# Kernel optimization log

Hardware: AMD Instinct MI355X
Metric: run time of the kernel (lower is better)

## Reference

```python
import jax, jax.numpy as jnp
import numpy as np

N_HEADS, N_KV, HEAD_DIM, D_MODEL, T_MAX = 16, 4, 64, 1024, 2048
GROUPS = N_HEADS // N_KV
EPS = 1e-6


def _rms_norm(x, w):
    # RMSNorm over last dim (head_dim), computed in fp32 like the torch module
    xf = x.astype(jnp.float32)
    r = jax.lax.rsqrt(jnp.mean(xf * xf, axis=-1, keepdims=True) + EPS)
    return (xf * r).astype(x.dtype) * w


def _apply_rope(x, cos, sin):
    # x: (B, H, T, D); cos/sin: (T_max, D/2)
    T = x.shape[2]
    c = cos[:T][None, None]  # (1,1,T,D/2)
    s = sin[:T][None, None]
    x1, x2 = jnp.split(x, 2, axis=-1)
    return jnp.concatenate([x1 * c - x2 * s, x2 * c + x1 * s], axis=-1)


def setup_inputs() -> dict:
    key = jax.random.key(0)
    ks = jax.random.split(key, 8)
    B, T = 2, 2048
    x = jax.random.normal(ks[0], (B, T, D_MODEL), dtype=jnp.float32)
    # realistic RoPE tables
    theta = 10000.0
    inv_freq = 1.0 / (theta ** (np.arange(0, HEAD_DIM, 2, dtype=np.float32) / HEAD_DIM))
    t = np.arange(T_MAX, dtype=np.float32)
    freqs = np.outer(t, inv_freq)  # (T_max, D/2)
    cos = jnp.asarray(np.cos(freqs))
    sin = jnp.asarray(np.sin(freqs))
    sd = 0.02
    wq = jax.random.normal(ks[1], (N_HEADS * HEAD_DIM, D_MODEL), dtype=jnp.float32) * sd
    wk = jax.random.normal(ks[2], (N_KV * HEAD_DIM, D_MODEL), dtype=jnp.float32) * sd
    wv = jax.random.normal(ks[3], (N_KV * HEAD_DIM, D_MODEL), dtype=jnp.float32) * sd
    wo = jax.random.normal(ks[4], (D_MODEL, N_HEADS * HEAD_DIM), dtype=jnp.float32) * sd
    qn_w = jnp.ones((HEAD_DIM,), dtype=jnp.float32)
    kn_w = jnp.ones((HEAD_DIM,), dtype=jnp.float32)
    return {"x": x, "cos": cos, "sin": sin, "wq": wq, "wk": wk, "wv": wv,
            "wo": wo, "qn_w": qn_w, "kn_w": kn_w}


def reference(x, cos, sin, wq, wk, wv, wo, qn_w, kn_w):
    B, T, _ = x.shape
    scale = HEAD_DIM ** -0.5
    # projections (torch Linear: y = x @ W.T)
    q = (x @ wq.T).reshape(B, T, N_HEADS, HEAD_DIM).transpose(0, 2, 1, 3)
    k = (x @ wk.T).reshape(B, T, N_KV, HEAD_DIM).transpose(0, 2, 1, 3)
    v = (x @ wv.T).reshape(B, T, N_KV, HEAD_DIM).transpose(0, 2, 1, 3)
    # qk RMSNorm
    q = _rms_norm(q, qn_w)
    k = _rms_norm(k, kn_w)
    # RoPE
    q = _apply_rope(q, cos, sin)
    k = _apply_rope(k, cos, sin)
    # GQA expansion: query head h uses kv head h // GROUPS
    k = jnp.repeat(k, GROUPS, axis=1)  # (B, H, T, D)
    v = jnp.repeat(v, GROUPS, axis=1)
    # causal SDPA
    scores = jnp.einsum('bhqd,bhkd->bhqk', q, k) * scale
    causal = jnp.tril(jnp.ones((T, T), dtype=bool))
    scores = jnp.where(causal, scores, jnp.finfo(scores.dtype).min)
    p = jax.nn.softmax(scores, axis=-1)
    out = jnp.einsum('bhqk,bhkd->bhqd', p, v)
    out = out.transpose(0, 2, 1, 3).reshape(B, T, N_HEADS * HEAD_DIM)
    return out @ wo.T
```

## Files before the change

kernel.cpp:

```cpp
#include <hip/hip_runtime.h>


typedef __bf16 bf16;
typedef __attribute__((ext_vector_type(4))) __bf16 bf16x4;
typedef __attribute__((ext_vector_type(8))) __bf16 bf16x8;
typedef __attribute__((ext_vector_type(4))) float f32x4;

#define MFMA(a, b, c) __builtin_amdgcn_mfma_f32_16x16x32_bf16((a), (b), (c), 0, 0, 0)
#define GLOAD_LDS16(g, l)                                        \
  __builtin_amdgcn_global_load_lds(                              \
      (const __attribute__((address_space(1))) void*)(g),        \
      (__attribute__((address_space(3))) void*)(l), 16, 0, 0)

__device__ __forceinline__ bool is_bf16_input(const void* cosRaw) {
  return ((const unsigned short*)cosRaw)[0] == 0x3F80;
}
__device__ __forceinline__ float rdval(const void* p, int idx, bool isbf) {
  return isbf ? (float)((const bf16*)p)[idx] : ((const float*)p)[idx];
}

__global__ __launch_bounds__(256) void convert_kernel(
    const void* __restrict__ x, const void* __restrict__ wq,
    const void* __restrict__ wk, const void* __restrict__ wv,
    const void* __restrict__ wo, bf16* __restrict__ dx,
    bf16* __restrict__ dw, const void* __restrict__ cosraw) {
  const bool isbf = is_bf16_input(cosraw);
  const int c = (int)blockIdx.x * 256 + (int)threadIdx.x;
  const void* src;
  int off;
  bf16* dst;
  int dc;
  if (c < 524288)      { src = x;  off = c;          dst = dx; dc = c; }
  else if (c < 655360) { src = wq; off = c - 524288; dst = dw; dc = c - 524288; }
  else if (c < 688128) { src = wk; off = c - 655360; dst = dw; dc = c - 524288; }
  else if (c < 720896) { src = wv; off = c - 688128; dst = dw; dc = c - 524288; }
  else                 { src = wo; off = c - 720896; dst = dw; dc = c - 524288; }
  bf16x8 o;
  if (isbf) {
    o = ((const bf16x8*)src)[off];
  } else {
    const float4* fp = (const float4*)src + (size_t)off * 2;
    float4 f0 = fp[0];
    float4 f1 = fp[1];
    o[0] = (bf16)f0.x; o[1] = (bf16)f0.y; o[2] = (bf16)f0.z; o[3] = (bf16)f0.w;
    o[4] = (bf16)f1.x; o[5] = (bf16)f1.y; o[6] = (bf16)f1.z; o[7] = (bf16)f1.w;
  }
  ((bf16x8*)dst)[dc] = o;
}

__global__ __launch_bounds__(256, 3) void proj_kernel(
    const bf16* __restrict__ xb, const bf16* __restrict__ wqb,
    const bf16* __restrict__ wkb, const bf16* __restrict__ wvb,
    bf16* __restrict__ qp, bf16* __restrict__ kp, bf16* __restrict__ vt,
    const void* __restrict__ cosraw, const void* __restrict__ sinraw,
    const void* __restrict__ qnraw, const void* __restrict__ knraw) {
  __shared__ bf16 As[128 * 64];
  __shared__ bf16 Bs[64 * 64];

  const int idx = (int)blockIdx.x;
  const int xcd = idx & 7;
  const int jj = idx >> 3;
  const int mb = (jj & 3) * 8 + xcd;
  const int nb = jj >> 2;
  const int n0 = nb * 64;
  const int m0 = mb * 128;

  const int tid = threadIdx.x;
  const int wave = tid >> 6;
  const int lane = tid & 63;
  const int q16 = lane & 15;
  const int quad = lane >> 4;
  const int srow = lane >> 3;
  const int csrc = (lane & 7) ^ srow;
  const int x7 = q16 & 7;

  const bf16* wsrc;
  int nr0;
  if (nb < 16)      { wsrc = wqb; nr0 = n0; }
  else if (nb < 20) { wsrc = wkb; nr0 = n0 - 1024; }
  else              { wsrc = wvb; nr0 = n0 - 1280; }

  f32x4 acc[2][4];
#pragma unroll
  for (int mf = 0; mf < 2; ++mf)
#pragma unroll
    for (int nt = 0; nt < 4; ++nt) acc[mf][nt] = (f32x4){0.f, 0.f, 0.f, 0.f};

  for (int kt = 0; kt < 16; ++kt) {
    const int ko = kt * 64;
#pragma unroll
    for (int i = 0; i < 4; ++i) {
      int rb = wave * 32 + i * 8;
      GLOAD_LDS16(&xb[(size_t)(m0 + rb + srow) * 1024 + ko + csrc * 8],
                  &As[rb * 64]);
    }
#pragma unroll
    for (int i = 0; i < 2; ++i) {
      int rb = wave * 16 + i * 8;
      GLOAD_LDS16(&wsrc[(size_t)(nr0 + rb + srow) * 1024 + ko + csrc * 8],
                  &Bs[rb * 64]);
    }
    __syncthreads();

    bf16x8 a[2][2], bfr[4][2];
#pragma unroll
    for (int mf = 0; mf < 2; ++mf) {
      const bf16* rp = &As[(wave * 32 + mf * 16 + q16) * 64];
      a[mf][0] = *(const bf16x8*)&rp[(quad ^ x7) * 8];
      a[mf][1] = *(const bf16x8*)&rp[((quad + 4) ^ x7) * 8];
    }
#pragma unroll
    for (int nt = 0; nt < 4; ++nt) {
      const bf16* rp = &Bs[(nt * 16 + q16) * 64];
      bfr[nt][0] = *(const bf16x8*)&rp[(quad ^ x7) * 8];
      bfr[nt][1] = *(const bf16x8*)&rp[((quad + 4) ^ x7) * 8];
    }
#pragma unroll
    for (int nt = 0; nt < 4; ++nt)
#pragma unroll
      for (int mf = 0; mf < 2; ++mf) {
        acc[mf][nt] = MFMA(a[mf][0], bfr[nt][0], acc[mf][nt]);
        acc[mf][nt] = MFMA(a[mf][1], bfr[nt][1], acc[mf][nt]);
      }
    __syncthreads();
  }

  if (nb < 20) {
    const bool isbf = is_bf16_input(cosraw);
    const void* nwp = (nb < 16) ? qnraw : knraw;
    const float osc = (nb < 16) ? 0.125f : 1.0f;
    float wd[4];
#pragma unroll
    for (int nt = 0; nt < 4; ++nt) wd[nt] = rdval(nwp, nt * 16 + q16, isbf);

#pragma unroll
    for (int mf = 0; mf < 2; ++mf) {
#pragma unroll
      for (int r = 0; r < 4; ++r) {
        float p = acc[mf][0][r] * acc[mf][0][r] + acc[mf][1][r] * acc[mf][1][r] +
                  acc[mf][2][r] * acc[mf][2][r] + acc[mf][3][r] * acc[mf][3][r];
#pragma unroll
        for (int off = 8; off >= 1; off >>= 1) p += __shfl_xor(p, off);
        float rms = rsqrtf(p * (1.0f / 64.0f) + 1e-6f);

        int row = m0 + wave * 32 + mf * 16 + quad * 4 + r;
        int t = row & 2047;
        float c0 = rdval(cosraw, t * 32 + q16, isbf);
        float c1 = rdval(cosraw, t * 32 + 16 + q16, isbf);
        float s0 = rdval(sinraw, t * 32 + q16, isbf);
        float s1 = rdval(sinraw, t * 32 + 16 + q16, isbf);

        float v0 = acc[mf][0][r] * rms * wd[0];
        float v1 = acc[mf][1][r] * rms * wd[1];
        float v2 = acc[mf][2][r] * rms * wd[2];
        float v3 = acc[mf][3][r] * rms * wd[3];

        bf16* op = (nb < 16) ? &qp[(size_t)row * 1024 + nb * 64]
                             : &kp[(size_t)row * 256 + (nb - 16) * 64];
        op[0 * 16 + q16] = (bf16)((v0 * c0 - v2 * s0) * osc);
        op[1 * 16 + q16] = (bf16)((v1 * c1 - v3 * s1) * osc);
        op[2 * 16 + q16] = (bf16)((v2 * c0 + v0 * s0) * osc);
        op[3 * 16 + q16] = (bf16)((v3 * c1 + v1 * s1) * osc);
      }
    }
  } else {
    const int vh = nb - 20;
    const int b = m0 >> 11;
    const int tbase = m0 & 2047;
#pragma unroll
    for (int mf = 0; mf < 2; ++mf)
#pragma unroll
      for (int nt = 0; nt < 4; ++nt)
#pragma unroll
        for (int r = 0; r < 4; ++r)
          As[(wave * 32 + mf * 16 + quad * 4 + r) * 64 + nt * 16 + q16] =
              (bf16)acc[mf][nt][r];
    __syncthreads();
#pragma unroll
    for (int rep = 0; rep < 4; ++rep) {
      int c = tid + 256 * rep;
      int d = c >> 4;
      int t8 = (c & 15) * 8;
      bf16x8 pk;
#pragma unroll
      for (int j = 0; j < 8; ++j) pk[j] = As[(t8 + j) * 64 + d];
      *(bf16x8*)&vt[(((size_t)(b * 4 + vh)) * 64 + d) * 2048 + tbase + t8] = pk;
    }
  }
}

__global__ __launch_bounds__(256, 4) void flash_kernel(
    const bf16* __restrict__ qp, const bf16* __restrict__ kp,
    const bf16* __restrict__ vt, bf16* __restrict__ attn) {
  const int qblk = blockIdx.z ? 31 - (int)blockIdx.x : (int)blockIdx.x;
  const int h = blockIdx.y;
  const int b = blockIdx.z;
  const int kvh = h >> 2;
  const int tid = threadIdx.x;
  const int wave = tid >> 6;
  const int lane = tid & 63;
  const int q16 = lane & 15;
  const int quad = lane >> 4;
  const int r7 = q16 & 7;
  const int t0 = qblk * 64 + wave * 16;

  __shared__ bf16 Ks[2][64 * 64];
  __shared__ bf16 Vs[2][64 * 64];
  __shared__ bf16 Pl[4][16 * 32];

  const bf16* qrow = qp + (((size_t)(b * 2048 + t0 + q16)) * 16 + h) * 64;
  bf16x8 qa0 = *(const bf16x8*)(qrow + quad * 8);
  bf16x8 qa1 = *(const bf16x8*)(qrow + 32 + quad * 8);

  bf16x8 ones;
#pragma unroll
  for (int j = 0; j < 8; ++j) ones[j] = (bf16)1.0f;

  f32x4 O[4], l4;
#pragma unroll
  for (int nt = 0; nt < 4; ++nt) O[nt] = (f32x4){0.f, 0.f, 0.f, 0.f};
  l4 = (f32x4){0.f, 0.f, 0.f, 0.f};

  const int ntile = qblk + 1;

  bf16x8 kr[2], vr[2];
  const int cr = tid * 2;
  const int krow = cr >> 3;
  const size_t kgbase = (((size_t)(b * 2048) + krow) * 4 + kvh) * 64;
  const size_t vgbase = ((size_t)(b * 4 + kvh) * 64 + krow) * 2048;

  auto gload = [&](int tk) {
#pragma unroll
    for (int rep = 0; rep < 2; ++rep) {
      int ch = (cr + rep) & 7;
      kr[rep] = *(const bf16x8*)&kp[kgbase + (size_t)(tk * 64) * 256 + ch * 8];
      vr[rep] = *(const bf16x8*)&vt[vgbase + tk * 64 + ch * 8];
    }
  };
  auto swrite = [&](int bb) {
#pragma unroll
    for (int rep = 0; rep < 2; ++rep) {
      int ch = (cr + rep) & 7;
      int pos = (ch ^ (krow & 7)) * 8;
      *(bf16x8*)&Ks[bb][krow * 64 + pos] = kr[rep];
      *(bf16x8*)&Vs[bb][krow * 64 + pos] = vr[rep];
    }
  };

  gload(0);

  for (int t = 0; t < ntile; ++t) {
    const int bb = t & 1;
    const int kbase = t * 64;
    swrite(bb);
    __syncthreads();
    if (t + 1 < ntile) gload(t + 1);

    f32x4 s[4];
#pragma unroll
    for (int kt = 0; kt < 4; ++kt) {
      const bf16* kr0 = &Ks[bb][(kt * 16 + q16) * 64];
      bf16x8 kb0 = *(const bf16x8*)&kr0[(quad ^ r7) * 8];
      bf16x8 kb1 = *(const bf16x8*)&kr0[((quad + 4) ^ r7) * 8];
      f32x4 z = (f32x4){0.f, 0.f, 0.f, 0.f};
      z = MFMA(kb0, qa0, z);
      z = MFMA(kb1, qa1, z);
      s[kt] = z;
    }

    if (kbase + 63 > t0) {
      const int q = t0 + q16;
#pragma unroll
      for (int kt = 0; kt < 4; ++kt) {
        int jt = kbase + kt * 16 + quad * 4;
#pragma unroll
        for (int r = 0; r < 4; ++r)
          if (jt + r > q) s[kt][r] = -1e30f;
      }
    }

#pragma unroll
    for (int kt = 0; kt < 4; ++kt)
#pragma unroll
      for (int r = 0; r < 4; ++r) s[kt][r] = __expf(s[kt][r] - 9.0f);

#pragma unroll
    for (int kh = 0; kh < 2; ++kh) {
#pragma unroll
      for (int ct = 0; ct < 2; ++ct) {
        const int kt = kh * 2 + ct;
        bf16x4 pk;
#pragma unroll
        for (int r = 0; r < 4; ++r) pk[r] = (bf16)s[kt][r];
        *(bf16x4*)&Pl[wave][q16 * 32 + ((ct * 4 + quad) ^ (q16 & 6)) * 4] = pk;
      }
      bf16x8 pa = *(const bf16x8*)&Pl[wave][q16 * 32 + ((quad * 2) ^ (q16 & 6)) * 4];
#pragma unroll
      for (int nt = 0; nt < 4; ++nt) {
        const bf16* vr0 = &Vs[bb][(nt * 16 + q16) * 64];
        bf16x8 vb = *(const bf16x8*)&vr0[((kh * 4 + quad) ^ r7) * 8];
        O[nt] = MFMA(pa, vb, O[nt]);
      }
      l4 = MFMA(pa, ones, l4);
    }
  }

  float inv[4];
#pragma unroll
  for (int r = 0; r < 4; ++r) inv[r] = 1.0f / l4[r];
#pragma unroll
  for (int nt = 0; nt < 4; ++nt)
#pragma unroll
    for (int r = 0; r < 4; ++r) {
      size_t o = (((size_t)(b * 2048 + t0 + quad * 4 + r)) * 16 + h) * 64 +
                 nt * 16 + q16;
      attn[o] = (bf16)(O[nt][r] * inv[r]);
    }
}

__global__ __launch_bounds__(256, 6) void gemm_o_kernel(
    const bf16* __restrict__ A, const bf16* __restrict__ W,
    void* __restrict__ C, const void* __restrict__ cosraw) {
  __shared__ bf16 As[64 * 64];
  __shared__ bf16 Bs[64 * 64];

  const int idx = (int)blockIdx.x;
  const int xcd = idx & 7;
  const int jj = idx >> 3;
  const int mb = (jj & 7) * 8 + xcd;
  const int nb = jj >> 3;
  const int n0 = nb * 64;
  const int m0 = mb * 64;

  const int tid = threadIdx.x;
  const int wave = tid >> 6;
  const int lane = tid & 63;
  const int q16 = lane & 15;
  const int quad = lane >> 4;
  const int srow = lane >> 3;
  const int csrc = (lane & 7) ^ srow;
  const int wm = wave * 16;
  const int x7 = q16 & 7;
  const bool isbf = is_bf16_input(cosraw);

  f32x4 acc[4];
#pragma unroll
  for (int nt = 0; nt < 4; ++nt) acc[nt] = (f32x4){0.f, 0.f, 0.f, 0.f};

  for (int kt = 0; kt < 16; ++kt) {
    const int ko = kt * 64;
#pragma unroll
    for (int i = 0; i < 2; ++i) {
      int rb = wave * 16 + i * 8;
      GLOAD_LDS16(&A[(size_t)(m0 + rb + srow) * 1024 + ko + csrc * 8],
                  &As[rb * 64]);
      GLOAD_LDS16(&W[(size_t)(n0 + rb + srow) * 1024 + ko + csrc * 8],
                  &Bs[rb * 64]);
    }
    __syncthreads();

    bf16x8 a0, a1, bfr[4][2];
    {
      const bf16* rp = &As[(wm + q16) * 64];
      a0 = *(const bf16x8*)&rp[(quad ^ x7) * 8];
      a1 = *(const bf16x8*)&rp[((quad + 4) ^ x7) * 8];
    }
#pragma unroll
    for (int nt = 0; nt < 4; ++nt) {
      const bf16* rp = &Bs[(nt * 16 + q16) * 64];
      bfr[nt][0] = *(const bf16x8*)&rp[(quad ^ x7) * 8];
      bfr[nt][1] = *(const bf16x8*)&rp[((quad + 4) ^ x7) * 8];
    }
#pragma unroll
    for (int nt = 0; nt < 4; ++nt) {
      acc[nt] = MFMA(a0, bfr[nt][0], acc[nt]);
      acc[nt] = MFMA(a1, bfr[nt][1], acc[nt]);
    }
    __syncthreads();
  }

#pragma unroll
  for (int nt = 0; nt < 4; ++nt)
#pragma unroll
    for (int r = 0; r < 4; ++r) {
      size_t idx2 = (size_t)(m0 + wm + quad * 4 + r) * 1024 + n0 + nt * 16 + q16;
      if (isbf) ((bf16*)C)[idx2] = (bf16)acc[nt][r];
      else      ((float*)C)[idx2] = acc[nt][r];
    }
}

extern "C" void kernel_launch(void* const* d_in, const int* in_sizes, int n_in,
                              void* d_out, int out_size, void* d_ws, size_t ws_size,
                              hipStream_t stream) {
  bf16* qp = (bf16*)d_ws;
  bf16* kp = qp + (size_t)4194304;
  bf16* vt = kp + (size_t)1048576;
  bf16* at = vt + (size_t)1048576;
  bf16* xb = at + (size_t)4194304;
  bf16* dw = xb + (size_t)4194304;

  bf16* wqb = dw;
  bf16* wkb = dw + (size_t)1048576;
  bf16* wvb = dw + (size_t)1310720;
  bf16* wob = dw + (size_t)1572864;

  convert_kernel<<<3328, 256, 0, stream>>>(
      d_in[0], d_in[3], d_in[4], d_in[5], d_in[6], xb, dw, d_in[1]);

  proj_kernel<<<768, 256, 0, stream>>>(
      xb, wqb, wkb, wvb, qp, kp, vt,
      d_in[1], d_in[2], d_in[7], d_in[8]);

  flash_kernel<<<dim3(32, 16, 2), 256, 0, stream>>>(qp, kp, vt, at);

  gemm_o_kernel<<<1024, 256, 0, stream>>>(at, wob, d_out, d_in[1]);
}
```

Baseline: 155.7 us.

## Share K/V tiles across two adjacent query blocks per 512-thread flash block

The flash attention kernel now launches 512-thread blocks, with each half handling one of two adjacent 64-row query blocks and both halves sharing the same double-buffered K/V shared-memory tiles. This halves the number of K/V global loads per query row and halves the grid size, while each thread now loads one chunk instead of two. The lower query group sits idle, apart from barriers, during the last KV tile. Larger blocks may reduce occupancy and add synchronisation cost.

```diff
diff --git a/kernel.cpp b/kernel.cpp
--- a/kernel.cpp
+++ b/kernel.cpp
@@ -189,24 +189,30 @@
   }
 }
 
-__global__ __launch_bounds__(256, 4) void flash_kernel(
+__global__ __launch_bounds__(512, 4) void flash_kernel(
     const bf16* __restrict__ qp, const bf16* __restrict__ kp,
     const bf16* __restrict__ vt, bf16* __restrict__ attn) {
-  const int qblk = blockIdx.z ? 31 - (int)blockIdx.x : (int)blockIdx.x;
-  const int h = blockIdx.y;
-  const int b = blockIdx.z;
+  const int x = (int)blockIdx.x;
+  const int h = (int)blockIdx.y;
+  const int b = (int)blockIdx.z;
+  const int p = b ? 15 - x : x;
   const int kvh = h >> 2;
-  const int tid = threadIdx.x;
+  const int tid = (int)threadIdx.x;
   const int wave = tid >> 6;
+  const int g = wave >> 2;
+  const int w4 = wave & 3;
   const int lane = tid & 63;
   const int q16 = lane & 15;
   const int quad = lane >> 4;
   const int r7 = q16 & 7;
-  const int t0 = qblk * 64 + wave * 16;
+  const int qblk = 2 * p + g;
+  const int t0 = qblk * 64 + w4 * 16;
+  const int NT = 2 * p + 2;
+  const int myNT = qblk + 1;
 
   __shared__ bf16 Ks[2][64 * 64];
   __shared__ bf16 Vs[2][64 * 64];
-  __shared__ bf16 Pl[4][16 * 32];
+  __shared__ bf16 Pl[8][16 * 32];
 
   const bf16* qrow = qp + (((size_t)(b * 2048 + t0 + q16)) * 16 + h) * 64;
   bf16x8 qa0 = *(const bf16x8*)(qrow + quad * 8);
@@ -221,87 +227,80 @@
   for (int nt = 0; nt < 4; ++nt) O[nt] = (f32x4){0.f, 0.f, 0.f, 0.f};
   l4 = (f32x4){0.f, 0.f, 0.f, 0.f};
 
-  const int ntile = qblk + 1;
-
-  bf16x8 kr[2], vr[2];
-  const int cr = tid * 2;
-  const int krow = cr >> 3;
+  bf16x8 kr, vr;
+  const int krow = tid >> 3;
+  const int ch = tid & 7;
   const size_t kgbase = (((size_t)(b * 2048) + krow) * 4 + kvh) * 64;
   const size_t vgbase = ((size_t)(b * 4 + kvh) * 64 + krow) * 2048;
 
   auto gload = [&](int tk) {
-#pragma unroll
-    for (int rep = 0; rep < 2; ++rep) {
-      int ch = (cr + rep) & 7;
-      kr[rep] = *(const bf16x8*)&kp[kgbase + (size_t)(tk * 64) * 256 + ch * 8];
-      vr[rep] = *(const bf16x8*)&vt[vgbase + tk * 64 + ch * 8];
-    }
+    kr = *(const bf16x8*)&kp[kgbase + (size_t)(tk * 64) * 256 + ch * 8];
+    vr = *(const bf16x8*)&vt[vgbase + tk * 64 + ch * 8];
   };
   auto swrite = [&](int bb) {
-#pragma unroll
-    for (int rep = 0; rep < 2; ++rep) {
-      int ch = (cr + rep) & 7;
-      int pos = (ch ^ (krow & 7)) * 8;
-      *(bf16x8*)&Ks[bb][krow * 64 + pos] = kr[rep];
-      *(bf16x8*)&Vs[bb][krow * 64 + pos] = vr[rep];
-    }
+    int pos = (ch ^ (krow & 7)) * 8;
+    *(bf16x8*)&Ks[bb][krow * 64 + pos] = kr;
+    *(bf16x8*)&Vs[bb][krow * 64 + pos] = vr;
   };
 
   gload(0);
 
-  for (int t = 0; t < ntile; ++t) {
+  for (int t = 0; t < NT; ++t) {
     const int bb = t & 1;
     const int kbase = t * 64;
     swrite(bb);
     __syncthreads();
-    if (t + 1 < ntile) gload(t + 1);
-
-    f32x4 s[4];
-#pragma unroll
-    for (int kt = 0; kt < 4; ++kt) {
-      const bf16* kr0 = &Ks[bb][(kt * 16 + q16) * 64];
-      bf16x8 kb0 = *(const bf16x8*)&kr0[(quad ^ r7) * 8];
-      bf16x8 kb1 = *(const bf16x8*)&kr0[((quad + 4) ^ r7) * 8];
-      f32x4 z = (f32x4){0.f, 0.f, 0.f, 0.f};
-      z = MFMA(kb0, qa0, z);
-      z = MFMA(kb1, qa1, z);
-      s[kt] = z;
-    }
-
-    if (kbase + 63 > t0) {
-      const int q = t0 + q16;
+    if (t + 1 < NT) gload(t + 1);
+
+    if (t < myNT) {
+      f32x4 s[4];
 #pragma unroll
       for (int kt = 0; kt < 4; ++kt) {
-        int jt = kbase + kt * 16 + quad * 4;
-#pragma unroll
-        for (int r = 0; r < 4; ++r)
-          if (jt + r > q) s[kt][r] = -1e30f;
+        const bf16* kr0 = &Ks[bb][(kt * 16 + q16) * 64];
+        bf16x8 kb0 = *(const bf16x8*)&kr0[(quad ^ r7) * 8];
+        bf16x8 kb1 = *(const bf16x8*)&kr0[((quad + 4) ^ r7) * 8];
+        f32x4 z = (f32x4){0.f, 0.f, 0.f, 0.f};
+        z = MFMA(kb0, qa0, z);
+        z = MFMA(kb1, qa1, z);
+        s[kt] = z;
       }
-    }
-
-#pragma unroll
-    for (int kt = 0; kt < 4; ++kt)
-#pragma unroll
-      for (int r = 0; r < 4; ++r) s[kt][r] = __expf(s[kt][r] - 9.0f);
-
-#pragma unroll
-    for (int kh = 0; kh < 2; ++kh) {
-#pragma unroll
-      for (int ct = 0; ct < 2; ++ct) {
-        const int kt = kh * 2 + ct;
-        bf16x4 pk;
-#pragma unroll
-        for (int r = 0; r < 4; ++r) pk[r] = (bf16)s[kt][r];
-        *(bf16x4*)&Pl[wave][q16 * 32 + ((ct * 4 + quad) ^ (q16 & 6)) * 4] = pk;
+
+      if (kbase + 63 > t0) {
+        const int q = t0 + q16;
+#pragma unroll
+        for (int kt = 0; kt < 4; ++kt) {
+          int jt = kbase + kt * 16 + quad * 4;
+#pragma unroll
+          for (int r = 0; r < 4; ++r)
+            if (jt + r > q) s[kt][r] = -1e30f;
+        }
       }
-      bf16x8 pa = *(const bf16x8*)&Pl[wave][q16 * 32 + ((quad * 2) ^ (q16 & 6)) * 4];
-#pragma unroll
-      for (int nt = 0; nt < 4; ++nt) {
-        const bf16* vr0 = &Vs[bb][(nt * 16 + q16) * 64];
-        bf16x8 vb = *(const bf16x8*)&vr0[((kh * 4 + quad) ^ r7) * 8];
-        O[nt] = MFMA(pa, vb, O[nt]);
+
+#pragma unroll
+      for (int kt = 0; kt < 4; ++kt)
+#pragma unroll
+        for (int r = 0; r < 4; ++r) s[kt][r] = __expf(s[kt][r] - 9.0f);
+
+#pragma unroll
+      for (int kh = 0; kh < 2; ++kh) {
+#pragma unroll
+        for (int ct = 0; ct < 2; ++ct) {
+          const int kt = kh * 2 + ct;
+          bf16x4 pk;
+#pragma unroll
+          for (int r = 0; r < 4; ++r) pk[r] = (bf16)s[kt][r];
+          *(bf16x4*)&Pl[wave][q16 * 32 + ((ct * 4 + quad) ^ (q16 & 6)) * 4] = pk;
+        }
+        bf16x8 pa =
+            *(const bf16x8*)&Pl[wave][q16 * 32 + ((quad * 2) ^ (q16 & 6)) * 4];
+#pragma unroll
+        for (int nt = 0; nt < 4; ++nt) {
+          const bf16* vr0 = &Vs[bb][(nt * 16 + q16) * 64];
+          bf16x8 vb = *(const bf16x8*)&vr0[((kh * 4 + quad) ^ r7) * 8];
+          O[nt] = MFMA(pa, vb, O[nt]);
+        }
+        l4 = MFMA(pa, ones, l4);
       }
-      l4 = MFMA(pa, ones, l4);
     }
   }
 
@@ -411,7 +410,7 @@
       xb, wqb, wkb, wvb, qp, kp, vt,
       d_in[1], d_in[2], d_in[7], d_in[8]);
 
-  flash_kernel<<<dim3(32, 16, 2), 256, 0, stream>>>(qp, kp, vt, at);
+  flash_kernel<<<dim3(16, 16, 2), 512, 0, stream>>>(qp, kp, vt, at);
 
   gemm_o_kernel<<<1024, 256, 0, stream>>>(at, wob, d_out, d_in[1]);
 }
```

Result: no change. 157.2 us (+0.9%).
